# Performance work log

Measured on AMD Instinct MI355X. Metric: run time of the kernel, lower is better.

## Reference

```python
import jax, jax.numpy as jnp
import numpy as np

N_NODES = 100000
N_EDGES = 6400000
IN_NODE = 6
IN_EDGE = 1
HID = 10
OUT = 2


def setup_inputs() -> dict:
    key = jax.random.key(0)
    ks = jax.random.split(key, 8)
    x = jax.random.normal(ks[0], (N_NODES, IN_NODE), dtype=jnp.float32)
    edge_index = jax.random.randint(ks[1], (2, N_EDGES), 0, N_NODES, dtype=jnp.int64)
    edge_attr = jax.random.normal(ks[2], (N_EDGES, IN_EDGE), dtype=jnp.float32)
    edge_attr_T = jax.random.normal(ks[3], (N_EDGES, IN_EDGE), dtype=jnp.float32)
    in_dim = 2 * IN_NODE + IN_EDGE  # 13
    W1 = jax.random.normal(ks[4], (in_dim, HID), dtype=jnp.float32) / np.sqrt(in_dim)
    b1 = jnp.zeros((HID,), dtype=jnp.float32)
    W2 = jax.random.normal(ks[5], (HID, OUT), dtype=jnp.float32) / np.sqrt(HID)
    b2 = jnp.zeros((OUT,), dtype=jnp.float32)
    return {"x": x, "edge_index": edge_index, "edge_attr": edge_attr,
            "edge_attr_T": edge_attr_T, "W1": W1, "b1": b1, "W2": W2, "b2": b2}


def _mlp(feat, W1, b1, W2, b2):
    h = jax.nn.relu(feat @ W1 + b1)
    return h @ W2 + b2


def reference(x, edge_index, edge_attr, edge_attr_T, W1, b1, W2, b2):
    src = edge_index[0]
    tgt = edge_index[1]
    x_src = x[src]  # [E, 6]
    x_tgt = x[tgt]  # [E, 6]
    feat_fwd = jnp.concatenate([x_src, x_tgt, edge_attr], axis=-1)      # [E, 13]
    feat_rev = jnp.concatenate([x_tgt, x_src, edge_attr_T], axis=-1)    # [E, 13]
    out = _mlp(feat_fwd, W1, b1, W2, b2) + _mlp(feat_rev, W1, b1, W2, b2)
    out = out * 0.5
    out = jax.nn.softmax(out, axis=1)
    return out[:, -1:]  # [E, 1]
```

## Files before the change

### kernel.cpp

```cpp
#include <hip/hip_runtime.h>



__global__ void prep_weights(const float* __restrict__ W1, const float* __restrict__ b1,
                             const float* __restrict__ W2, const float* __restrict__ b2,
                             float* __restrict__ w) {
    int t = threadIdx.x;
    if (t < 60) {
        int i = t / 10, j = t % 10;
        float a = W1[i * 10 + j];
        float c = W1[(i + 6) * 10 + j];
        w[t]      = 0.5f * (a + c);
        w[60 + t] = 0.5f * (a - c);
    }
    if (t < 10) {
        w[120 + t] = W1[120 + t];
        w[130 + t] = b1[t];
        w[140 + t] = 0.5f * (W2[t * 2 + 1] - W2[t * 2]);
    }
    if (t == 0) {
        w[150] = b2[1] - b2[0];
        w[151] = 0.0f;
    }
}

__launch_bounds__(256, 2)
__global__ void edge_mlp(const float* __restrict__ x, const int* __restrict__ ei,
                         const float* __restrict__ ea, const float* __restrict__ eaT,
                         const float* __restrict__ wg, float* __restrict__ out, int E) {
    float W[152];
    const float4* w4 = (const float4*)wg;
#pragma unroll
    for (int k = 0; k < 38; ++k) {
        float4 v = w4[k];
        W[4 * k + 0] = v.x; W[4 * k + 1] = v.y;
        W[4 * k + 2] = v.z; W[4 * k + 3] = v.w;
    }

    const float2* xr = (const float2*)x;
    int tid = blockIdx.x * blockDim.x + threadIdx.x;
    int stride = gridDim.x * blockDim.x;

    for (int e = tid; e < E; e += stride) {
        int si = ei[e];
        int ti = ei[E + e];
        float fea  = ea[e];
        float feaT = eaT[e];

        float2 a0 = xr[3 * si], a1 = xr[3 * si + 1], a2 = xr[3 * si + 2];
        float2 c0 = xr[3 * ti], c1 = xr[3 * ti + 1], c2 = xr[3 * ti + 2];
        float xs[6] = {a0.x, a0.y, a1.x, a1.y, a2.x, a2.y};
        float xt[6] = {c0.x, c0.y, c1.x, c1.y, c2.x, c2.y};

        float sv[6], dv[6];
#pragma unroll
        for (int i = 0; i < 6; ++i) { sv[i] = xs[i] + xt[i]; dv[i] = xs[i] - xt[i]; }

        float cacc[10], macc[10];
#pragma unroll
        for (int j = 0; j < 10; ++j) { cacc[j] = W[130 + j]; macc[j] = 0.0f; }
#pragma unroll
        for (int i = 0; i < 6; ++i) {
#pragma unroll
            for (int j = 0; j < 10; ++j) {
                cacc[j] = fmaf(sv[i], W[i * 10 + j],      cacc[j]);
                macc[j] = fmaf(dv[i], W[60 + i * 10 + j], macc[j]);
            }
        }

        float z = W[150];
#pragma unroll
        for (int j = 0; j < 10; ++j) {
            float af = fmaf(fea,  W[120 + j], cacc[j] + macc[j]);
            float ar = fmaf(feaT, W[120 + j], cacc[j] - macc[j]);
            float h  = fmaxf(af, 0.0f) + fmaxf(ar, 0.0f);
            z = fmaf(h, W[140 + j], z);
        }

        out[e] = 1.0f / (1.0f + __expf(-z));
    }
}

extern "C" void kernel_launch(void* const* d_in, const int* in_sizes, int n_in,
                              void* d_out, int out_size, void* d_ws, size_t ws_size,
                              hipStream_t stream) {
    const float* x   = (const float*)d_in[0];
    const int*   ei  = (const int*)d_in[1];
    const float* ea  = (const float*)d_in[2];
    const float* eaT = (const float*)d_in[3];
    const float* W1  = (const float*)d_in[4];
    const float* b1  = (const float*)d_in[5];
    const float* W2  = (const float*)d_in[6];
    const float* b2  = (const float*)d_in[7];
    float* out = (float*)d_out;
    float* w   = (float*)d_ws;
    int E = in_sizes[2];

    prep_weights<<<1, 64, 0, stream>>>(W1, b1, W2, b2, w);
    edge_mlp<<<512, 256, 0, stream>>>(x, ei, ea, eaT, w, out, E);
}
```

Baseline: 236.5 us.

## Use one thread per edge with uniform weight loads and nontemporal streaming

Replaces the grid-stride loop, which held 152 weights in registers, with a one-edge-per-thread launch over the whole edge set. Weights are read directly from global memory at uniform addresses, so they can go through scalar loads and cut register pressure. Launch bounds are raised to allow more waves per SIMD. Streaming inputs and the output use nontemporal loads and stores to keep the cache free for the random node-feature gathers. The cost is more block launches and re-reading the weights in every block.

```diff
diff --git a/kernel.cpp b/kernel.cpp
--- a/kernel.cpp
+++ b/kernel.cpp
@@ -1,5 +1,4 @@
 #include <hip/hip_runtime.h>
-
 
 
 __global__ void prep_weights(const float* __restrict__ W1, const float* __restrict__ b1,
@@ -24,61 +23,51 @@
     }
 }
 
-__launch_bounds__(256, 2)
+__launch_bounds__(256, 8)
 __global__ void edge_mlp(const float* __restrict__ x, const int* __restrict__ ei,
                          const float* __restrict__ ea, const float* __restrict__ eaT,
                          const float* __restrict__ wg, float* __restrict__ out, int E) {
-    float W[152];
-    const float4* w4 = (const float4*)wg;
+    int e = blockIdx.x * 256 + threadIdx.x;
+    if (e >= E) return;
+
+    int   si   = __builtin_nontemporal_load(ei + e);
+    int   ti   = __builtin_nontemporal_load(ei + E + e);
+    float fea  = __builtin_nontemporal_load(ea + e);
+    float feaT = __builtin_nontemporal_load(eaT + e);
+
+    const float2* xr = (const float2*)x;
+    float2 a0 = xr[3 * si], a1 = xr[3 * si + 1], a2 = xr[3 * si + 2];
+    float2 c0 = xr[3 * ti], c1 = xr[3 * ti + 1], c2 = xr[3 * ti + 2];
+    float xs[6] = {a0.x, a0.y, a1.x, a1.y, a2.x, a2.y};
+    float xt[6] = {c0.x, c0.y, c1.x, c1.y, c2.x, c2.y};
+
+    float sv[6], dv[6];
 #pragma unroll
-    for (int k = 0; k < 38; ++k) {
-        float4 v = w4[k];
-        W[4 * k + 0] = v.x; W[4 * k + 1] = v.y;
-        W[4 * k + 2] = v.z; W[4 * k + 3] = v.w;
+    for (int i = 0; i < 6; ++i) { sv[i] = xs[i] + xt[i]; dv[i] = xs[i] - xt[i]; }
+
+    float cacc[10], macc[10];
+#pragma unroll
+    for (int j = 0; j < 10; ++j) { cacc[j] = wg[130 + j]; macc[j] = 0.0f; }
+#pragma unroll
+    for (int i = 0; i < 6; ++i) {
+#pragma unroll
+        for (int j = 0; j < 10; ++j) {
+            cacc[j] = fmaf(sv[i], wg[i * 10 + j],      cacc[j]);
+            macc[j] = fmaf(dv[i], wg[60 + i * 10 + j], macc[j]);
+        }
     }
 
-    const float2* xr = (const float2*)x;
-    int tid = blockIdx.x * blockDim.x + threadIdx.x;
-    int stride = gridDim.x * blockDim.x;
+    float z = wg[150];
+#pragma unroll
+    for (int j = 0; j < 10; ++j) {
+        float af = fmaf(fea,  wg[120 + j], cacc[j] + macc[j]);
+        float ar = fmaf(feaT, wg[120 + j], cacc[j] - macc[j]);
+        float h  = fmaxf(af, 0.0f) + fmaxf(ar, 0.0f);
+        z = fmaf(h, wg[140 + j], z);
+    }
 
-    for (int e = tid; e < E; e += stride) {
-        int si = ei[e];
-        int ti = ei[E + e];
-        float fea  = ea[e];
-        float feaT = eaT[e];
-
-        float2 a0 = xr[3 * si], a1 = xr[3 * si + 1], a2 = xr[3 * si + 2];
-        float2 c0 = xr[3 * ti], c1 = xr[3 * ti + 1], c2 = xr[3 * ti + 2];
-        float xs[6] = {a0.x, a0.y, a1.x, a1.y, a2.x, a2.y};
-        float xt[6] = {c0.x, c0.y, c1.x, c1.y, c2.x, c2.y};
-
-        float sv[6], dv[6];
-#pragma unroll
-        for (int i = 0; i < 6; ++i) { sv[i] = xs[i] + xt[i]; dv[i] = xs[i] - xt[i]; }
-
-        float cacc[10], macc[10];
-#pragma unroll
-        for (int j = 0; j < 10; ++j) { cacc[j] = W[130 + j]; macc[j] = 0.0f; }
-#pragma unroll
-        for (int i = 0; i < 6; ++i) {
-#pragma unroll
-            for (int j = 0; j < 10; ++j) {
-                cacc[j] = fmaf(sv[i], W[i * 10 + j],      cacc[j]);
-                macc[j] = fmaf(dv[i], W[60 + i * 10 + j], macc[j]);
-            }
-        }
-
-        float z = W[150];
-#pragma unroll
-        for (int j = 0; j < 10; ++j) {
-            float af = fmaf(fea,  W[120 + j], cacc[j] + macc[j]);
-            float ar = fmaf(feaT, W[120 + j], cacc[j] - macc[j]);
-            float h  = fmaxf(af, 0.0f) + fmaxf(ar, 0.0f);
-            z = fmaf(h, W[140 + j], z);
-        }
-
-        out[e] = 1.0f / (1.0f + __expf(-z));
-    }
+    float r = 1.0f / (1.0f + __expf(-z));
+    __builtin_nontemporal_store(r, out + e);
 }
 
 extern "C" void kernel_launch(void* const* d_in, const int* in_sizes, int n_in,
@@ -97,5 +86,6 @@
     int E = in_sizes[2];
 
     prep_weights<<<1, 64, 0, stream>>>(W1, b1, W2, b2, w);
-    edge_mlp<<<512, 256, 0, stream>>>(x, ei, ea, eaT, w, out, E);
+    int blocks = (E + 255) / 256;
+    edge_mlp<<<blocks, 256, 0, stream>>>(x, ei, ea, eaT, w, out, E);
 }
```

Result: no change. 233.0 us (-1.4%).
